# Performance work log

Measured on AMD Instinct MI355X. Metric: run time of the kernel, lower is better.

The kernel has to match this reference:

```python
import jax, jax.numpy as jnp
import numpy as np

EMB = 512
H = 8
DK = EMB // H          # 64
MAX_SEQ = 768
TOPK = MAX_SEQ // 2    # 384


def setup_inputs() -> dict:
    key = jax.random.key(0)
    ks = jax.random.split(key, 16)
    B, S, E = 1, MAX_SEQ, EMB

    def w(k, shape):
        return jax.random.normal(k, shape, dtype=jnp.float32) * 0.02

    return {
        "x": jax.random.normal(ks[0], (B, S, E), dtype=jnp.float32),
        # main attention projections (Linear weights stored as (in, out))
        "Wq": w(ks[1], (E, E)), "bq": w(ks[2], (E,)),
        "Wk": w(ks[3], (E, E)), "bk": w(ks[4], (E,)),
        "Wv": w(ks[5], (E, E)), "bv": w(ks[6], (E,)),
        "Wo": w(ks[7], (E, E)), "bo": w(ks[8], (E,)),
        # indexer projections: wq -> (E, H*DK)=(E,E), wk -> (E, DK), weights_proj -> (E, H)
        "iq_W": w(ks[9], (E, H * DK)), "iq_b": w(ks[10], (H * DK,)),
        "ik_W": w(ks[11], (E, DK)),    "ik_b": w(ks[12], (DK,)),
        "wp_W": w(ks[13], (E, H)),     "wp_b": w(ks[14], (H,)),
    }


def reference(x, Wq, bq, Wk, bk, Wv, bv, Wo, bo, iq_W, iq_b, ik_W, ik_b, wp_W, wp_b):
    B, S, E = x.shape
    scaling = 1.0 / np.sqrt(DK)

    def split_heads(z):  # (B,S,E) -> (B,H,S,DK)
        return z.reshape(B, S, H, DK).transpose(0, 2, 1, 3)

    Q = split_heads(x @ Wq + bq)
    K = split_heads(x @ Wk + bk)
    V = split_heads(x @ Wv + bv)

    # --- indexer: per-token relevance scores ---
    q_idx = (x @ iq_W + iq_b).reshape(B, S, H, DK).transpose(0, 2, 1, 3)  # (B,H,S,DK)
    k_idx = x @ ik_W + ik_b                                               # (B,S,DK)
    w_idx = x @ wp_W + wp_b                                               # (B,S,H)
    score = jax.nn.relu(jnp.einsum('bhsd,btd->bhst', q_idx, k_idx))       # (B,H,S,S)
    indexer_score = jnp.einsum('bhst,bsh->bst', score, w_idx)             # (B,S,S)

    # --- top-k selection (set-equivalent to argpartition in the original) ---
    topk_idx = jax.lax.top_k(indexer_score, TOPK)[1]                      # (B,S,TOPK) int32

    # --- gather sparse K/V per query token ---
    def gather_b(Zb, idxb):  # Zb:(H,S,DK), idxb:(S,TOPK) -> (H,S,TOPK,DK)
        return Zb[:, idxb, :]
    K_s = jax.vmap(gather_b)(K, topk_idx)  # (B,H,S,TOPK,DK)
    V_s = jax.vmap(gather_b)(V, topk_idx)  # (B,H,S,TOPK,DK)

    # --- sparse attention over selected tokens ---
    sc = jnp.einsum('bhsd,bhskd->bhsk', Q, K_s) * scaling  # (B,H,S,TOPK)
    wts = jax.nn.softmax(sc, axis=-1)
    attn = jnp.einsum('bhsk,bhskd->bhsd', wts, V_s)        # (B,H,S,DK)

    out = attn.transpose(0, 2, 1, 3).reshape(B, S, E) @ Wo + bo
    return out
```

## Files before the change

kernel.cpp:

```cpp
#include <hip/hip_runtime.h>
#include <hip/hip_bf16.h>
#include <math.h>

#define S 768
#define E 512
#define H 8
#define DK 64
#define TOPK 384

typedef short bf16x8 __attribute__((ext_vector_type(8)));
typedef float f32x4 __attribute__((ext_vector_type(4)));

__device__ __forceinline__ unsigned short f2bf(float x) {
  unsigned u = __float_as_uint(x);
  unsigned r = u + 0x7FFFu + ((u >> 16) & 1u);
  return (unsigned short)(r >> 16);
}
__device__ __forceinline__ float bf2f(unsigned short h) {
  return __uint_as_float(((unsigned)h) << 16);
}
__device__ __forceinline__ void split1(float x, unsigned short& h, unsigned short& l) {
  h = f2bf(x);
  l = f2bf(x - bf2f(h));
}

__device__ __forceinline__ void mfma3(f32x4& d, bf16x8 ah, bf16x8 al,
                                      bf16x8 bh, bf16x8 bl) {
  d = __builtin_amdgcn_mfma_f32_16x16x32_bf16(ah, bh, d, 0, 0, 0);
  d = __builtin_amdgcn_mfma_f32_16x16x32_bf16(ah, bl, d, 0, 0, 0);
  d = __builtin_amdgcn_mfma_f32_16x16x32_bf16(al, bh, d, 0, 0, 0);
}
__device__ __forceinline__ void mfma2(f32x4& d, bf16x8 ah, bf16x8 al, bf16x8 bh) {
  d = __builtin_amdgcn_mfma_f32_16x16x32_bf16(ah, bh, d, 0, 0, 0);
  d = __builtin_amdgcn_mfma_f32_16x16x32_bf16(al, bh, d, 0, 0, 0);
}

__device__ __forceinline__ bf16x8 ldfrag(const unsigned short* p) {
  return *reinterpret_cast<const bf16x8*>(p);
}

struct PrepTab {
  const float* src[8];
  unsigned short* hi[8];
  unsigned short* lo[8];
};

__global__ __launch_bounds__(256) void prep_kernel(PrepTab t) {
  const int seg = blockIdx.z;
  const int rows = (seg == 0) ? 768 : 512;
  const int cols = (seg == 5) ? 64 : ((seg == 6) ? 8 : 512);
  const int tx = (seg == 6) ? 2 : ((cols + 31) >> 5);
  const int ty = rows >> 5;
  if ((int)blockIdx.x >= tx || (int)blockIdx.y >= ty) return;
  const int r0 = blockIdx.y * 32, c0 = blockIdx.x * 32;
  const int tid = threadIdx.x;
  const int rl = tid >> 3, c4 = (tid & 7) << 2;
  const float* src = t.src[seg];
  if (seg == 0) {
    float4 v = *(const float4*)(src + (size_t)(r0 + rl) * cols + c0 + c4);
    unsigned short h[4], l[4];
    split1(v.x, h[0], l[0]); split1(v.y, h[1], l[1]);
    split1(v.z, h[2], l[2]); split1(v.w, h[3], l[3]);
    size_t off = (size_t)(r0 + rl) * cols + c0 + c4;
    *(ushort4*)(t.hi[seg] + off) = make_ushort4(h[0], h[1], h[2], h[3]);
    *(ushort4*)(t.lo[seg] + off) = make_ushort4(l[0], l[1], l[2], l[3]);
  } else {
    __shared__ float ts[32][33];
    #pragma unroll
    for (int j = 0; j < 4; ++j) {
      int c = c4 + j;
      ts[rl][c] = (c0 + c < cols) ? src[(size_t)(r0 + rl) * cols + c0 + c] : 0.0f;
    }
    __syncthreads();
    float v0 = ts[c4 + 0][rl], v1 = ts[c4 + 1][rl];
    float v2 = ts[c4 + 2][rl], v3 = ts[c4 + 3][rl];
    unsigned short h[4], l[4];
    split1(v0, h[0], l[0]); split1(v1, h[1], l[1]);
    split1(v2, h[2], l[2]); split1(v3, h[3], l[3]);
    size_t off = (size_t)(c0 + rl) * 512 + r0 + c4;
    *(ushort4*)(t.hi[seg] + off) = make_ushort4(h[0], h[1], h[2], h[3]);
    *(ushort4*)(t.lo[seg] + off) = make_ushort4(l[0], l[1], l[2], l[3]);
  }
}

struct ProjTab {
  const unsigned short* whi[6];
  const unsigned short* wlo[6];
  const float* bias[6];
};

__global__ __launch_bounds__(256) void proj_mfma_kernel(
    const unsigned short* __restrict__ Xhi, const unsigned short* __restrict__ Xlo,
    ProjTab pt,
    unsigned short* __restrict__ Qhi, unsigned short* __restrict__ Qlo,
    unsigned short* __restrict__ Khi, unsigned short* __restrict__ Klo,
    unsigned short* __restrict__ VThi,
    unsigned short* __restrict__ QIhi, unsigned short* __restrict__ QIlo,
    unsigned short* __restrict__ KIhi, unsigned short* __restrict__ KIlo,
    float* __restrict__ WI) {
  __shared__ __align__(16) unsigned short Ah[64][72];
  __shared__ __align__(16) unsigned short Al[64][72];
  __shared__ __align__(16) unsigned short Bh[64][72];
  __shared__ __align__(16) unsigned short Bl[64][72];
  const int bx = blockIdx.x;
  int seg, nt;
  if (bx < 32) { seg = bx >> 3; nt = bx & 7; }
  else         { seg = 4 + (bx - 32); nt = 0; }
  const int m0 = blockIdx.y * 64;
  const int n0 = nt * 64;
  const int tid = threadIdx.x;
  const int lane = tid & 63;
  const int wave = tid >> 6;
  const int mq = (wave >> 1) << 5;
  const int nq = (wave & 1) << 5;
  const int l15 = lane & 15;
  const int q8 = (lane >> 4) << 3;
  const int q4 = (lane >> 4) << 2;
  const unsigned short* Whi = pt.whi[seg];
  const unsigned short* Wlo = pt.wlo[seg];

  const int mm0 = tid >> 3,          kc0 = (tid & 7) << 3;
  const int mm1 = (tid + 256) >> 3,  kc1 = ((tid + 256) & 7) << 3;
  const size_t ga0 = (size_t)(m0 + mm0) * 512 + kc0;
  const size_t gb0 = (size_t)(n0 + mm0) * 512 + kc0;
  const size_t ga1 = (size_t)(m0 + mm1) * 512 + kc1;
  const size_t gb1 = (size_t)(n0 + mm1) * 512 + kc1;

  bf16x8 rah0 = ldfrag(Xhi + ga0), ral0 = ldfrag(Xlo + ga0);
  bf16x8 rbh0 = ldfrag(Whi + gb0), rbl0 = ldfrag(Wlo + gb0);
  bf16x8 rah1 = ldfrag(Xhi + ga1), ral1 = ldfrag(Xlo + ga1);
  bf16x8 rbh1 = ldfrag(Whi + gb1), rbl1 = ldfrag(Wlo + gb1);

  f32x4 acc[2][2] = {};
  for (int cc = 0; cc < 8; ++cc) {
    *(bf16x8*)&Ah[mm0][kc0] = rah0;
    *(bf16x8*)&Al[mm0][kc0] = ral0;
    *(bf16x8*)&Bh[mm0][kc0] = rbh0;
    *(bf16x8*)&Bl[mm0][kc0] = rbl0;
    *(bf16x8*)&Ah[mm1][kc1] = rah1;
    *(bf16x8*)&Al[mm1][kc1] = ral1;
    *(bf16x8*)&Bh[mm1][kc1] = rbh1;
    *(bf16x8*)&Bl[mm1][kc1] = rbl1;
    if (cc < 7) {
      const size_t o = (size_t)(cc + 1) << 6;
      rah0 = ldfrag(Xhi + ga0 + o); ral0 = ldfrag(Xlo + ga0 + o);
      rbh0 = ldfrag(Whi + gb0 + o); rbl0 = ldfrag(Wlo + gb0 + o);
      rah1 = ldfrag(Xhi + ga1 + o); ral1 = ldfrag(Xlo + ga1 + o);
      rbh1 = ldfrag(Whi + gb1 + o); rbl1 = ldfrag(Wlo + gb1 + o);
    }
    __syncthreads();
    #pragma unroll
    for (int ki = 0; ki < 64; ki += 32) {
      const int kk = ki + q8;
      bf16x8 ah0 = *(const bf16x8*)&Ah[mq + l15][kk];
      bf16x8 al0 = *(const bf16x8*)&Al[mq + l15][kk];
      bf16x8 ah1 = *(const bf16x8*)&Ah[mq + 16 + l15][kk];
      bf16x8 al1 = *(const bf16x8*)&Al[mq + 16 + l15][kk];
      bf16x8 bh0 = *(const bf16x8*)&Bh[nq + l15][kk];
      bf16x8 bl0 = *(const bf16x8*)&Bl[nq + l15][kk];
      bf16x8 bh1 = *(const bf16x8*)&Bh[nq + 16 + l15][kk];
      bf16x8 bl1 = *(const bf16x8*)&Bl[nq + 16 + l15][kk];
      mfma3(acc[0][0], ah0, al0, bh0, bl0);
      mfma3(acc[0][1], ah0, al0, bh1, bl1);
      mfma3(acc[1][0], ah1, al1, bh0, bl0);
      mfma3(acc[1][1], ah1, al1, bh1, bl1);
    }
    __syncthreads();
  }

  const float* bias = pt.bias[seg];
  #pragma unroll
  for (int ntt = 0; ntt < 2; ++ntt) {
    const int nloc = n0 + nq + ntt * 16 + l15;
    const float bv = (seg == 5 && nloc >= 8) ? 0.0f : bias[nloc];
    #pragma unroll
    for (int mt = 0; mt < 2; ++mt) {
      #pragma unroll
      for (int r = 0; r < 4; ++r) {
        const int m = m0 + mq + mt * 16 + q4 + r;
        const float v = acc[mt][ntt][r] + bv;
        unsigned short h16, l16;
        if (seg == 0) {
          split1(v, h16, l16);
          Qhi[(size_t)m * 512 + nloc] = h16;
          Qlo[(size_t)m * 512 + nloc] = l16;
        } else if (seg == 1) {
          const int hh = nloc >> 6, dd = nloc & 63;
          split1(v, h16, l16);
          Khi[((size_t)hh * S + m) * 64 + dd] = h16;
          Klo[((size_t)hh * S + m) * 64 + dd] = l16;
        } else if (seg == 2) {
          VThi[((size_t)(nloc >> 6) * 64 + (nloc & 63)) * S + m] = f2bf(v);
        } else if (seg == 3) {
          split1(v, h16, l16);
          QIhi[(size_t)m * 512 + nloc] = h16;
          QIlo[(size_t)m * 512 + nloc] = l16;
        } else if (seg == 4) {
          split1(v, h16, l16);
          KIhi[(size_t)m * 64 + nloc] = h16;
          KIlo[(size_t)m * 64 + nloc] = l16;
        } else {
          if (nloc < 8) WI[(size_t)m * 8 + nloc] = v;
        }
      }
    }
  }
}

__global__ __launch_bounds__(256) void indexer_mfma_kernel(
    const unsigned short* __restrict__ QIhi, const unsigned short* __restrict__ QIlo,
    const unsigned short* __restrict__ KIhi, const unsigned short* __restrict__ KIlo,
    const float* __restrict__ WI, float* __restrict__ ISC) {
  __shared__ __align__(16) unsigned short Qh[32][136];
  __shared__ __align__(16) unsigned short Ql[32][136];
  __shared__ float wis[32][8];
  const int s0 = blockIdx.y * 32, t0 = blockIdx.x * 64;
  const int tid = threadIdx.x;
  const int lane = tid & 63;
  const int wave = tid >> 6;
  const int mq = (wave >> 1) << 4;
  const int nqb = (wave & 1) << 5;
  const int l15 = lane & 15;
  const int q8 = (lane >> 4) << 3;
  const int q4 = (lane >> 4) << 2;
  wis[tid >> 3][tid & 7] = WI[(size_t)(s0 + (tid >> 3)) * 8 + (tid & 7)];

  const size_t brow0 = (size_t)(t0 + nqb + l15) * 64;
  const size_t brow1 = (size_t)(t0 + nqb + 16 + l15) * 64;
  bf16x8 kfh[2][2], kfl[2][2];
  #pragma unroll
  for (int kk = 0; kk < 2; ++kk) {
    const int kb = kk * 32 + q8;
    kfh[kk][0] = ldfrag(KIhi + brow0 + kb);
    kfl[kk][0] = ldfrag(KIlo + brow0 + kb);
    kfh[kk][1] = ldfrag(KIhi + brow1 + kb);
    kfl[kk][1] = ldfrag(KIlo + brow1 + kb);
  }

  const int smm = tid >> 3;
  const int skc = (tid & 7) << 4;
  const size_t qbase = (size_t)(s0 + smm) * 512 + skc;
  bf16x8 rq0 = ldfrag(QIhi + qbase);
  bf16x8 rq1 = ldfrag(QIhi + qbase + 8);
  bf16x8 rq2 = ldfrag(QIlo + qbase);
  bf16x8 rq3 = ldfrag(QIlo + qbase + 8);

  float accI[2][4] = {};
  for (int hp = 0; hp < 4; ++hp) {
    __syncthreads();
    *(bf16x8*)&Qh[smm][skc]     = rq0;
    *(bf16x8*)&Qh[smm][skc + 8] = rq1;
    *(bf16x8*)&Ql[smm][skc]     = rq2;
    *(bf16x8*)&Ql[smm][skc + 8] = rq3;
    if (hp < 3) {
      const size_t g = qbase + (size_t)(hp + 1) * 128;
      rq0 = ldfrag(QIhi + g);
      rq1 = ldfrag(QIhi + g + 8);
      rq2 = ldfrag(QIlo + g);
      rq3 = ldfrag(QIlo + g + 8);
    }
    __syncthreads();
    #pragma unroll
    for (int hh = 0; hh < 2; ++hh) {
      const int h = hp * 2 + hh;
      f32x4 d[2] = {};
      #pragma unroll
      for (int kk = 0; kk < 2; ++kk) {
        const int ka = hh * 64 + kk * 32 + q8;
        bf16x8 ah = *(const bf16x8*)&Qh[mq + l15][ka];
        bf16x8 al = *(const bf16x8*)&Ql[mq + l15][ka];
        mfma3(d[0], ah, al, kfh[kk][0], kfl[kk][0]);
        mfma3(d[1], ah, al, kfh[kk][1], kfl[kk][1]);
      }
      #pragma unroll
      for (int r = 0; r < 4; ++r) {
        const float w = wis[mq + q4 + r][h];
        accI[0][r] = fmaf(fmaxf(d[0][r], 0.0f), w, accI[0][r]);
        accI[1][r] = fmaf(fmaxf(d[1][r], 0.0f), w, accI[1][r]);
      }
    }
  }
  #pragma unroll
  for (int ntt = 0; ntt < 2; ++ntt)
    #pragma unroll
    for (int r = 0; r < 4; ++r)
      ISC[(size_t)(s0 + mq + q4 + r) * S + t0 + nqb + ntt * 16 + l15] = accI[ntt][r];
}

__global__ __launch_bounds__(256) void topk_kernel(
    const float* __restrict__ ISC, unsigned* __restrict__ Mask,
    float* __restrict__ Sum, float* __restrict__ ATTacc) {
  __shared__ unsigned ordv[768];
  __shared__ int hist[256];
  __shared__ int gsum[16];
  __shared__ int sc[256];
  __shared__ unsigned mw[24];
  __shared__ unsigned sh_prefix;
  __shared__ int sh_R;
  const int s = blockIdx.x;
  const int tid = threadIdx.x;
  for (int i = tid; i < 768; i += 256) {
    float f = ISC[s * 768 + i] + 0.0f;
    unsigned u = __float_as_uint(f);
    ordv[i] = (u & 0x80000000u) ? ~u : (u | 0x80000000u);
  }
  {
    const float4 z4 = {0.0f, 0.0f, 0.0f, 0.0f};
    if (tid < 128) *(float4*)(ATTacc + (size_t)s * 512 + tid * 4) = z4;
  }
  if (tid < 24) mw[tid] = 0u;
  if (tid < H) Sum[tid * S + s] = 0.0f;
  if (tid == 0) { sh_prefix = 0u; sh_R = TOPK; }
  __syncthreads();
  for (int pass = 0; pass < 4; ++pass) {
    const int shift = 24 - pass * 8;
    hist[tid] = 0;
    __syncthreads();
    const unsigned pm = (pass == 0) ? 0u : (0xFFFFFFFFu << (shift + 8));
    const unsigned pref = sh_prefix;
    for (int i = tid; i < 768; i += 256) {
      unsigned o = ordv[i];
      if ((o & pm) == pref) atomicAdd(&hist[(o >> shift) & 255], 1);
    }
    __syncthreads();
    if (tid < 16) {
      int t = 0;
      #pragma unroll
      for (int k = 0; k < 16; ++k) t += hist[tid * 16 + k];
      gsum[tid] = t;
    }
    __syncthreads();
    if (tid == 0) {
      int R = sh_R;
      int G = 0;
      int g = 15;
      for (; g > 0; --g) {
        if (G + gsum[g] >= R) break;
        G += gsum[g];
      }
      int b = 15;
      for (; b > 0; --b) {
        int c = hist[g * 16 + b];
        if (G + c >= R) break;
        G += c;
      }
      sh_prefix = sh_prefix | ((unsigned)(g * 16 + b) << shift);
      sh_R = R - G;
    }
    __syncthreads();
  }
  const unsigned thr = sh_prefix;
  const int need_eq = sh_R;
  const int base = tid * 3;
  unsigned o0 = ordv[base], o1 = ordv[base + 1], o2 = ordv[base + 2];
  int c = (o0 == thr) + (o1 == thr) + (o2 == thr);
  sc[tid] = c;
  __syncthreads();
  for (int off = 1; off < 256; off <<= 1) {
    int v = (tid >= off) ? sc[tid - off] : 0;
    __syncthreads();
    sc[tid] += v;
    __syncthreads();
  }
  int rank = sc[tid] - c;
  if (o0 > thr || (o0 == thr && rank < need_eq))
    atomicOr(&mw[base >> 5], 1u << (base & 31));
  if (o0 == thr) ++rank;
  if (o1 > thr || (o1 == thr && rank < need_eq))
    atomicOr(&mw[(base + 1) >> 5], 1u << ((base + 1) & 31));
  if (o1 == thr) ++rank;
  if (o2 > thr || (o2 == thr && rank < need_eq))
    atomicOr(&mw[(base + 2) >> 5], 1u << ((base + 2) & 31));
  __syncthreads();
  if (tid < 24) Mask[s * 24 + tid] = mw[tid];
}

__global__ __launch_bounds__(512) void sattn_kernel(
    const unsigned short* __restrict__ Qhi, const unsigned short* __restrict__ Qlo,
    const unsigned short* __restrict__ Khi, const unsigned short* __restrict__ Klo,
    const unsigned short* __restrict__ VThi,
    const unsigned* __restrict__ Mask, float* __restrict__ ATTacc,
    float* __restrict__ Sum) {
  __shared__ __align__(16) unsigned short Ksh[64][72];
  __shared__ __align__(16) unsigned short Ksl[64][72];
  __shared__ __align__(16) unsigned short Vsh[64][72];
  __shared__ __align__(16) unsigned short Pshi[64][72];
  __shared__ __align__(16) unsigned short Pslo[64][72];
  __shared__ unsigned msk[64][6];
  __shared__ float rsumf[64];
  const int ks = blockIdx.x;
  const int s0 = blockIdx.y * 64;
  const int h  = blockIdx.z;
  const int tid = threadIdx.x;
  const int lane = tid & 63;
  const int wave = tid >> 6;
  const int l15 = lane & 15;
  const int q8 = (lane >> 4) << 3;
  const int q4 = (lane >> 4) << 2;
  const int mq = (wave >> 1) << 4;
  const int nqq = (wave & 1) << 4;
  const int db = (wave & 1) << 5;

  if (tid < 384) msk[tid & 63][tid >> 6] =
      Mask[(size_t)(s0 + (tid & 63)) * 24 + ks * 6 + (tid >> 6)];
  if (tid < 64) rsumf[tid] = 0.0f;

  const size_t qrow = (size_t)(s0 + mq + l15) * 512 + h * 64;
  bf16x8 qh0 = ldfrag(Qhi + qrow + 0 + q8);
  bf16x8 ql0 = ldfrag(Qlo + qrow + 0 + q8);
  bf16x8 qh1 = ldfrag(Qhi + qrow + 32 + q8);
  bf16x8 ql1 = ldfrag(Qlo + qrow + 32 + q8);

  const int tr = tid >> 3;
  const int kc = (tid & 7) << 3;
  const size_t gkbase = ((size_t)h * S + ks * 192 + tr) * 64 + kc;
  const size_t gvbase = ((size_t)h * 64 + tr) * S + ks * 192 + kc;
  bf16x8 rkh = ldfrag(Khi + gkbase);
  bf16x8 rkl = ldfrag(Klo + gkbase);
  bf16x8 rv  = ldfrag(VThi + gvbase);

  f32x4 oacc[2] = {};
  for (int ct = 0; ct < 3; ++ct) {
    __syncthreads();
    *(bf16x8*)&Ksh[tr][kc] = rkh;
    *(bf16x8*)&Ksl[tr][kc] = rkl;
    *(bf16x8*)&Vsh[tr][kc] = rv;
    if (ct < 2) {
      rkh = ldfrag(Khi + gkbase + (size_t)(ct + 1) * 4096);
      rkl = ldfrag(Klo + gkbase + (size_t)(ct + 1) * 4096);
      rv  = ldfrag(VThi + gvbase + (size_t)(ct + 1) * 64);
    }
    __syncthreads();
    float esum[4] = {0.0f, 0.0f, 0.0f, 0.0f};
    #pragma unroll
    for (int cp = 0; cp < 2; ++cp) {
      const int tcol = nqq + cp * 32;
      f32x4 d = {0.0f, 0.0f, 0.0f, 0.0f};
      bf16x8 bh0 = *(const bf16x8*)&Ksh[tcol + l15][q8];
      bf16x8 bl0 = *(const bf16x8*)&Ksl[tcol + l15][q8];
      bf16x8 bh1 = *(const bf16x8*)&Ksh[tcol + l15][32 + q8];
      bf16x8 bl1 = *(const bf16x8*)&Ksl[tcol + l15][32 + q8];
      mfma3(d, qh0, ql0, bh0, bl0);
      mfma3(d, qh1, ql1, bh1, bl1);
      const int tl = ct * 64 + tcol + l15;
      #pragma unroll
      for (int r = 0; r < 4; ++r) {
        const int srow = mq + q4 + r;
        const unsigned w = msk[srow][tl >> 5];
        float e = ((w >> (tl & 31)) & 1u) ? __expf(d[r] * 0.125f) : 0.0f;
        unsigned short h16, l16;
        split1(e, h16, l16);
        Pshi[srow][tcol + l15] = h16;
        Pslo[srow][tcol + l15] = l16;
        esum[r] += e;
      }
    }
    float v0 = esum[0], v1 = esum[1], v2 = esum[2], v3 = esum[3];
    #pragma unroll
    for (int off = 1; off < 16; off <<= 1) {
      v0 += __shfl_xor(v0, off);
      v1 += __shfl_xor(v1, off);
      v2 += __shfl_xor(v2, off);
      v3 += __shfl_xor(v3, off);
    }
    if (l15 == 0) {
      atomicAdd(&rsumf[mq + q4 + 0], v0);
      atomicAdd(&rsumf[mq + q4 + 1], v1);
      atomicAdd(&rsumf[mq + q4 + 2], v2);
      atomicAdd(&rsumf[mq + q4 + 3], v3);
    }
    __syncthreads();
    #pragma unroll
    for (int kk = 0; kk < 64; kk += 32) {
      bf16x8 pah = *(const bf16x8*)&Pshi[mq + l15][kk + q8];
      bf16x8 pal = *(const bf16x8*)&Pslo[mq + l15][kk + q8];
      #pragma unroll
      for (int dt = 0; dt < 2; ++dt) {
        bf16x8 vbh = *(const bf16x8*)&Vsh[db + dt * 16 + l15][kk + q8];
        mfma2(oacc[dt], pah, pal, vbh);
      }
    }
  }
  #pragma unroll
  for (int dt = 0; dt < 2; ++dt) {
    const int dd = db + dt * 16 + l15;
    #pragma unroll
    for (int r = 0; r < 4; ++r) {
      const int s = s0 + mq + q4 + r;
      atomicAdd(&ATTacc[(size_t)s * E + h * DK + dd], oacc[dt][r]);
    }
  }
  __syncthreads();
  if (tid < 64) atomicAdd(&Sum[(size_t)h * S + s0 + tid], rsumf[tid]);
}

__global__ __launch_bounds__(512) void out_mfma_kernel(
    const float* __restrict__ ATTacc, const float* __restrict__ Sum,
    const unsigned short* __restrict__ WoThi,
    const float* __restrict__ bo, float* __restrict__ out) {
  __shared__ float AccL[16][65];
  __shared__ float ivs[16][8];
  __shared__ __align__(16) unsigned short Ahi[16][520];
  __shared__ __align__(16) unsigned short Alo[16][520];
  const int tid512 = threadIdx.x;
  const int wave8 = tid512 >> 6;
  const int z = wave8 >> 2;
  const int wave = wave8 & 3;
  const int lane = tid512 & 63;
  const int m0 = blockIdx.y * 16;
  const int n0 = blockIdx.x * 64 + wave * 16;
  const int l15 = lane & 15;
  const int q8 = (lane >> 4) << 3;
  const int q4 = (lane >> 4) << 2;
  if (tid512 < 128) {
    const int r = tid512 >> 3, hh = tid512 & 7;
    ivs[r][hh] = 1.0f / Sum[(size_t)hh * S + m0 + r];
  }
  __syncthreads();
  {
    const int row = tid512 >> 5;
    const int kb = (tid512 & 31) << 4;
    const float inv = ivs[row][kb >> 6];
    const float* src = ATTacc + (size_t)(m0 + row) * 512 + kb;
    float4 a0 = *(const float4*)(src);
    float4 a1 = *(const float4*)(src + 4);
    float4 a2 = *(const float4*)(src + 8);
    float4 a3 = *(const float4*)(src + 12);
    float v[16] = {a0.x, a0.y, a0.z, a0.w, a1.x, a1.y, a1.z, a1.w,
                   a2.x, a2.y, a2.z, a2.w, a3.x, a3.y, a3.z, a3.w};
    #pragma unroll
    for (int i = 0; i < 16; ++i) {
      unsigned short hh, ll;
      split1(v[i] * inv, hh, ll);
      Ahi[row][kb + i] = hh;
      Alo[row][kb + i] = ll;
    }
  }
  __syncthreads();
  const size_t brow = (size_t)(n0 + l15) * 512;
  f32x4 acc = {};
  #pragma unroll
  for (int it = 0; it < 8; ++it) {
    const int ko = (z << 8) + (it << 5) + q8;
    bf16x8 ah = *(const bf16x8*)&Ahi[l15][ko];
    bf16x8 al = *(const bf16x8*)&Alo[l15][ko];
    bf16x8 bh = ldfrag(WoThi + brow + ko);
    mfma2(acc, ah, al, bh);
  }
  if (z == 1) {
    #pragma unroll
    for (int r = 0; r < 4; ++r)
      AccL[q4 + r][wave * 16 + l15] = acc[r];
  }
  __syncthreads();
  if (z == 0) {
    const int n = n0 + l15;
    const float bv = bo[n];
    #pragma unroll
    for (int r = 0; r < 4; ++r)
      out[(size_t)(m0 + q4 + r) * 512 + n] =
          acc[r] + AccL[q4 + r][wave * 16 + l15] + bv;
  }
}

extern "C" void kernel_launch(void* const* d_in, const int* in_sizes, int n_in,
                              void* d_out, int out_size, void* d_ws, size_t ws_size,
                              hipStream_t stream) {
  const float* x    = (const float*)d_in[0];
  const float* Wq   = (const float*)d_in[1];
  const float* bq   = (const float*)d_in[2];
  const float* Wk   = (const float*)d_in[3];
  const float* bk   = (const float*)d_in[4];
  const float* Wv   = (const float*)d_in[5];
  const float* bv   = (const float*)d_in[6];
  const float* Wo   = (const float*)d_in[7];
  const float* bo   = (const float*)d_in[8];
  const float* iqW  = (const float*)d_in[9];
  const float* iqb  = (const float*)d_in[10];
  const float* ikW  = (const float*)d_in[11];
  const float* ikb  = (const float*)d_in[12];
  const float* wpW  = (const float*)d_in[13];
  const float* wpb  = (const float*)d_in[14];

  float* ws = (float*)d_ws;
  float* WI   = ws;
  float* ISC  = WI + S * H;
  unsigned* Mask = (unsigned*)(ISC + S * S);
  float* Sum  = (float*)(Mask + S * 24);
  float* ATTacc = Sum + H * S;
  unsigned short* u = (unsigned short*)(ATTacc + S * E);
  unsigned short* Xhi  = u;             u += S * E;
  unsigned short* Xlo  = u;             u += S * E;
  unsigned short* Qhi  = u;             u += S * E;
  unsigned short* Qlo  = u;             u += S * E;
  unsigned short* Khi  = u;             u += S * E;
  unsigned short* Klo  = u;             u += S * E;
  unsigned short* VThi = u;             u += S * E;
  unsigned short* QIhi = u;             u += S * E;
  unsigned short* QIlo = u;             u += S * E;
  unsigned short* KIhi = u;             u += S * DK;
  unsigned short* KIlo = u;             u += S * DK;
  unsigned short* WTq_hi = u;           u += E * E;
  unsigned short* WTk_hi = u;           u += E * E;
  unsigned short* WTv_hi = u;           u += E * E;
  unsigned short* WTiq_hi = u;          u += E * E;
  unsigned short* WTik_hi = u;          u += 64 * E;
  unsigned short* WTwp_hi = u;          u += 64 * E;
  unsigned short* WTo_hi = u;           u += E * E;
  unsigned short* WTq_lo = u;           u += E * E;
  unsigned short* WTk_lo = u;           u += E * E;
  unsigned short* WTv_lo = u;           u += E * E;
  unsigned short* WTiq_lo = u;          u += E * E;
  unsigned short* WTik_lo = u;          u += 64 * E;
  unsigned short* WTwp_lo = u;          u += 64 * E;
  unsigned short* WTo_lo = u;           u += E * E;

  PrepTab prep;
  prep.src[0] = x;    prep.hi[0] = Xhi;     prep.lo[0] = Xlo;
  prep.src[1] = Wq;   prep.hi[1] = WTq_hi;  prep.lo[1] = WTq_lo;
  prep.src[2] = Wk;   prep.hi[2] = WTk_hi;  prep.lo[2] = WTk_lo;
  prep.src[3] = Wv;   prep.hi[3] = WTv_hi;  prep.lo[3] = WTv_lo;
  prep.src[4] = iqW;  prep.hi[4] = WTiq_hi; prep.lo[4] = WTiq_lo;
  prep.src[5] = ikW;  prep.hi[5] = WTik_hi; prep.lo[5] = WTik_lo;
  prep.src[6] = wpW;  prep.hi[6] = WTwp_hi; prep.lo[6] = WTwp_lo;
  prep.src[7] = Wo;   prep.hi[7] = WTo_hi;  prep.lo[7] = WTo_lo;

  ProjTab pt;
  pt.whi[0] = WTq_hi;  pt.wlo[0] = WTq_lo;  pt.bias[0] = bq;
  pt.whi[1] = WTk_hi;  pt.wlo[1] = WTk_lo;  pt.bias[1] = bk;
  pt.whi[2] = WTv_hi;  pt.wlo[2] = WTv_lo;  pt.bias[2] = bv;
  pt.whi[3] = WTiq_hi; pt.wlo[3] = WTiq_lo; pt.bias[3] = iqb;
  pt.whi[4] = WTik_hi; pt.wlo[4] = WTik_lo; pt.bias[4] = ikb;
  pt.whi[5] = WTwp_hi; pt.wlo[5] = WTwp_lo; pt.bias[5] = wpb;

  prep_kernel<<<dim3(16, 24, 8), dim3(256), 0, stream>>>(prep);
  proj_mfma_kernel<<<dim3(34, S / 64), dim3(256), 0, stream>>>(
      Xhi, Xlo, pt, Qhi, Qlo, Khi, Klo, VThi, QIhi, QIlo, KIhi, KIlo, WI);
  indexer_mfma_kernel<<<dim3(S / 64, S / 32), dim3(256), 0, stream>>>(
      QIhi, QIlo, KIhi, KIlo, WI, ISC);
  topk_kernel<<<dim3(S), dim3(256), 0, stream>>>(ISC, Mask, Sum, ATTacc);
  sattn_kernel<<<dim3(4, S / 64, H), dim3(512), 0, stream>>>(
      Qhi, Qlo, Khi, Klo, VThi, Mask, ATTacc, Sum);
  out_mfma_kernel<<<dim3(8, 48), dim3(512), 0, stream>>>(
      ATTacc, Sum, WTo_hi, bo, (float*)d_out);
}
```

Measured before the change: 139.5 us.

## Double-buffer LDS tiles, use wave-shuffle scan, and load K/V fragments directly

The projection and indexer kernels now double-buffer their shared-memory tiles, which cuts one barrier per k-step and lets global prefetch run further ahead. The top-k rank scan replaces a barrier-heavy shared-memory Hillis-Steele scan with per-wave shuffle scans plus a small cross-wave combine. The sparse attention kernel drops its LDS staging of K and V, loads MFMA fragments straight from global memory, double-buffers the P tile, and defers the row-sum reduction to the end. The price is more LDS per block in some kernels and uncoalesced direct global loads in the attention kernel.

Result: slower. 147.0 us (+5.3%).

```diff
diff --git a/kernel.cpp b/kernel.cpp
--- a/kernel.cpp
+++ b/kernel.cpp
@@ -98,10 +98,10 @@
     unsigned short* __restrict__ QIhi, unsigned short* __restrict__ QIlo,
     unsigned short* __restrict__ KIhi, unsigned short* __restrict__ KIlo,
     float* __restrict__ WI) {
-  __shared__ __align__(16) unsigned short Ah[64][72];
-  __shared__ __align__(16) unsigned short Al[64][72];
-  __shared__ __align__(16) unsigned short Bh[64][72];
-  __shared__ __align__(16) unsigned short Bl[64][72];
+  __shared__ __align__(16) unsigned short Ah[2][64][72];
+  __shared__ __align__(16) unsigned short Al[2][64][72];
+  __shared__ __align__(16) unsigned short Bh[2][64][72];
+  __shared__ __align__(16) unsigned short Bl[2][64][72];
   const int bx = blockIdx.x;
   int seg, nt;
   if (bx < 32) { seg = bx >> 3; nt = bx & 7; }
@@ -130,36 +130,44 @@
   bf16x8 rbh0 = ldfrag(Whi + gb0), rbl0 = ldfrag(Wlo + gb0);
   bf16x8 rah1 = ldfrag(Xhi + ga1), ral1 = ldfrag(Xlo + ga1);
   bf16x8 rbh1 = ldfrag(Whi + gb1), rbl1 = ldfrag(Wlo + gb1);
+  *(bf16x8*)&Ah[0][mm0][kc0] = rah0;  *(bf16x8*)&Al[0][mm0][kc0] = ral0;
+  *(bf16x8*)&Bh[0][mm0][kc0] = rbh0;  *(bf16x8*)&Bl[0][mm0][kc0] = rbl0;
+  *(bf16x8*)&Ah[0][mm1][kc1] = rah1;  *(bf16x8*)&Al[0][mm1][kc1] = ral1;
+  *(bf16x8*)&Bh[0][mm1][kc1] = rbh1;  *(bf16x8*)&Bl[0][mm1][kc1] = rbl1;
+  rah0 = ldfrag(Xhi + ga0 + 64); ral0 = ldfrag(Xlo + ga0 + 64);
+  rbh0 = ldfrag(Whi + gb0 + 64); rbl0 = ldfrag(Wlo + gb0 + 64);
+  rah1 = ldfrag(Xhi + ga1 + 64); ral1 = ldfrag(Xlo + ga1 + 64);
+  rbh1 = ldfrag(Whi + gb1 + 64); rbl1 = ldfrag(Wlo + gb1 + 64);
+  __syncthreads();
 
   f32x4 acc[2][2] = {};
   for (int cc = 0; cc < 8; ++cc) {
-    *(bf16x8*)&Ah[mm0][kc0] = rah0;
-    *(bf16x8*)&Al[mm0][kc0] = ral0;
-    *(bf16x8*)&Bh[mm0][kc0] = rbh0;
-    *(bf16x8*)&Bl[mm0][kc0] = rbl0;
-    *(bf16x8*)&Ah[mm1][kc1] = rah1;
-    *(bf16x8*)&Al[mm1][kc1] = ral1;
-    *(bf16x8*)&Bh[mm1][kc1] = rbh1;
-    *(bf16x8*)&Bl[mm1][kc1] = rbl1;
+    const int cur = cc & 1;
     if (cc < 7) {
-      const size_t o = (size_t)(cc + 1) << 6;
+      const int nb = 1 - cur;
+      *(bf16x8*)&Ah[nb][mm0][kc0] = rah0;  *(bf16x8*)&Al[nb][mm0][kc0] = ral0;
+      *(bf16x8*)&Bh[nb][mm0][kc0] = rbh0;  *(bf16x8*)&Bl[nb][mm0][kc0] = rbl0;
+      *(bf16x8*)&Ah[nb][mm1][kc1] = rah1;  *(bf16x8*)&Al[nb][mm1][kc1] = ral1;
+      *(bf16x8*)&Bh[nb][mm1][kc1] = rbh1;  *(bf16x8*)&Bl[nb][mm1][kc1] = rbl1;
+    }
+    if (cc < 6) {
+      const size_t o = (size_t)(cc + 2) << 6;
       rah0 = ldfrag(Xhi + ga0 + o); ral0 = ldfrag(Xlo + ga0 + o);
       rbh0 = ldfrag(Whi + gb0 + o); rbl0 = ldfrag(Wlo + gb0 + o);
       rah1 = ldfrag(Xhi + ga1 + o); ral1 = ldfrag(Xlo + ga1 + o);
       rbh1 = ldfrag(Whi + gb1 + o); rbl1 = ldfrag(Wlo + gb1 + o);
     }
-    __syncthreads();
     #pragma unroll
     for (int ki = 0; ki < 64; ki += 32) {
       const int kk = ki + q8;
-      bf16x8 ah0 = *(const bf16x8*)&Ah[mq + l15][kk];
-      bf16x8 al0 = *(const bf16x8*)&Al[mq + l15][kk];
-      bf16x8 ah1 = *(const bf16x8*)&Ah[mq + 16 + l15][kk];
-      bf16x8 al1 = *(const bf16x8*)&Al[mq + 16 + l15][kk];
-      bf16x8 bh0 = *(const bf16x8*)&Bh[nq + l15][kk];
-      bf16x8 bl0 = *(const bf16x8*)&Bl[nq + l15][kk];
-      bf16x8 bh1 = *(const bf16x8*)&Bh[nq + 16 + l15][kk];
-      bf16x8 bl1 = *(const bf16x8*)&Bl[nq + 16 + l15][kk];
+      bf16x8 ah0 = *(const bf16x8*)&Ah[cur][mq + l15][kk];
+      bf16x8 al0 = *(const bf16x8*)&Al[cur][mq + l15][kk];
+      bf16x8 ah1 = *(const bf16x8*)&Ah[cur][mq + 16 + l15][kk];
+      bf16x8 al1 = *(const bf16x8*)&Al[cur][mq + 16 + l15][kk];
+      bf16x8 bh0 = *(const bf16x8*)&Bh[cur][nq + l15][kk];
+      bf16x8 bl0 = *(const bf16x8*)&Bl[cur][nq + l15][kk];
+      bf16x8 bh1 = *(const bf16x8*)&Bh[cur][nq + 16 + l15][kk];
+      bf16x8 bl1 = *(const bf16x8*)&Bl[cur][nq + 16 + l15][kk];
       mfma3(acc[0][0], ah0, al0, bh0, bl0);
       mfma3(acc[0][1], ah0, al0, bh1, bl1);
       mfma3(acc[1][0], ah1, al1, bh0, bl0);
@@ -211,8 +219,8 @@
     const unsigned short* __restrict__ QIhi, const unsigned short* __restrict__ QIlo,
     const unsigned short* __restrict__ KIhi, const unsigned short* __restrict__ KIlo,
     const float* __restrict__ WI, float* __restrict__ ISC) {
-  __shared__ __align__(16) unsigned short Qh[32][136];
-  __shared__ __align__(16) unsigned short Ql[32][136];
+  __shared__ __align__(16) unsigned short Qh[2][32][136];
+  __shared__ __align__(16) unsigned short Ql[2][32][136];
   __shared__ float wis[32][8];
   const int s0 = blockIdx.y * 32, t0 = blockIdx.x * 64;
   const int tid = threadIdx.x;
@@ -244,22 +252,33 @@
   bf16x8 rq1 = ldfrag(QIhi + qbase + 8);
   bf16x8 rq2 = ldfrag(QIlo + qbase);
   bf16x8 rq3 = ldfrag(QIlo + qbase + 8);
+  *(bf16x8*)&Qh[0][smm][skc]     = rq0;
+  *(bf16x8*)&Qh[0][smm][skc + 8] = rq1;
+  *(bf16x8*)&Ql[0][smm][skc]     = rq2;
+  *(bf16x8*)&Ql[0][smm][skc + 8] = rq3;
+  rq0 = ldfrag(QIhi + qbase + 128);
+  rq1 = ldfrag(QIhi + qbase + 136);
+  rq2 = ldfrag(QIlo + qbase + 128);
+  rq3 = ldfrag(QIlo + qbase + 136);
+  __syncthreads();
 
   float accI[2][4] = {};
   for (int hp = 0; hp < 4; ++hp) {
-    __syncthreads();
-    *(bf16x8*)&Qh[smm][skc]     = rq0;
-    *(bf16x8*)&Qh[smm][skc + 8] = rq1;
-    *(bf16x8*)&Ql[smm][skc]     = rq2;
-    *(bf16x8*)&Ql[smm][skc + 8] = rq3;
+    const int cur = hp & 1;
     if (hp < 3) {
-      const size_t g = qbase + (size_t)(hp + 1) * 128;
+      const int nb = 1 - cur;
+      *(bf16x8*)&Qh[nb][smm][skc]     = rq0;
+      *(bf16x8*)&Qh[nb][smm][skc + 8] = rq1;
+      *(bf16x8*)&Ql[nb][smm][skc]     = rq2;
+      *(bf16x8*)&Ql[nb][smm][skc + 8] = rq3;
+    }
+    if (hp < 2) {
+      const size_t g = qbase + (size_t)(hp + 2) * 128;
       rq0 = ldfrag(QIhi + g);
       rq1 = ldfrag(QIhi + g + 8);
       rq2 = ldfrag(QIlo + g);
       rq3 = ldfrag(QIlo + g + 8);
     }
-    __syncthreads();
     #pragma unroll
     for (int hh = 0; hh < 2; ++hh) {
       const int h = hp * 2 + hh;
@@ -267,8 +286,8 @@
       #pragma unroll
       for (int kk = 0; kk < 2; ++kk) {
         const int ka = hh * 64 + kk * 32 + q8;
-        bf16x8 ah = *(const bf16x8*)&Qh[mq + l15][ka];
-        bf16x8 al = *(const bf16x8*)&Ql[mq + l15][ka];
+        bf16x8 ah = *(const bf16x8*)&Qh[cur][mq + l15][ka];
+        bf16x8 al = *(const bf16x8*)&Ql[cur][mq + l15][ka];
         mfma3(d[0], ah, al, kfh[kk][0], kfl[kk][0]);
         mfma3(d[1], ah, al, kfh[kk][1], kfl[kk][1]);
       }
@@ -279,6 +298,7 @@
         accI[1][r] = fmaf(fmaxf(d[1][r], 0.0f), w, accI[1][r]);
       }
     }
+    __syncthreads();
   }
   #pragma unroll
   for (int ntt = 0; ntt < 2; ++ntt)
@@ -293,7 +313,7 @@
   __shared__ unsigned ordv[768];
   __shared__ int hist[256];
   __shared__ int gsum[16];
-  __shared__ int sc[256];
+  __shared__ int wtot[4];
   __shared__ unsigned mw[24];
   __shared__ unsigned sh_prefix;
   __shared__ int sh_R;
@@ -354,15 +374,19 @@
   const int base = tid * 3;
   unsigned o0 = ordv[base], o1 = ordv[base + 1], o2 = ordv[base + 2];
   int c = (o0 == thr) + (o1 == thr) + (o2 == thr);
-  sc[tid] = c;
-  __syncthreads();
-  for (int off = 1; off < 256; off <<= 1) {
-    int v = (tid >= off) ? sc[tid - off] : 0;
-    __syncthreads();
-    sc[tid] += v;
-    __syncthreads();
-  }
-  int rank = sc[tid] - c;
+  const int lane = tid & 63, wv = tid >> 6;
+  int sum = c;
+  #pragma unroll
+  for (int off = 1; off < 64; off <<= 1) {
+    int v = __shfl_up(sum, off);
+    if (lane >= off) sum += v;
+  }
+  if (lane == 63) wtot[wv] = sum;
+  __syncthreads();
+  int rank = sum - c;
+  if (wv > 0) rank += wtot[0];
+  if (wv > 1) rank += wtot[1];
+  if (wv > 2) rank += wtot[2];
   if (o0 > thr || (o0 == thr && rank < need_eq))
     atomicOr(&mw[base >> 5], 1u << (base & 31));
   if (o0 == thr) ++rank;
@@ -381,11 +405,8 @@
     const unsigned short* __restrict__ VThi,
     const unsigned* __restrict__ Mask, float* __restrict__ ATTacc,
     float* __restrict__ Sum) {
-  __shared__ __align__(16) unsigned short Ksh[64][72];
-  __shared__ __align__(16) unsigned short Ksl[64][72];
-  __shared__ __align__(16) unsigned short Vsh[64][72];
-  __shared__ __align__(16) unsigned short Pshi[64][72];
-  __shared__ __align__(16) unsigned short Pslo[64][72];
+  __shared__ __align__(16) unsigned short Pshi[2][64][72];
+  __shared__ __align__(16) unsigned short Pslo[2][64][72];
   __shared__ unsigned msk[64][6];
   __shared__ float rsumf[64];
   const int ks = blockIdx.x;
@@ -406,43 +427,38 @@
   if (tid < 64) rsumf[tid] = 0.0f;
 
   const size_t qrow = (size_t)(s0 + mq + l15) * 512 + h * 64;
-  bf16x8 qh0 = ldfrag(Qhi + qrow + 0 + q8);
-  bf16x8 ql0 = ldfrag(Qlo + qrow + 0 + q8);
+  bf16x8 qh0 = ldfrag(Qhi + qrow + q8);
+  bf16x8 ql0 = ldfrag(Qlo + qrow + q8);
   bf16x8 qh1 = ldfrag(Qhi + qrow + 32 + q8);
   bf16x8 ql1 = ldfrag(Qlo + qrow + 32 + q8);
 
-  const int tr = tid >> 3;
-  const int kc = (tid & 7) << 3;
-  const size_t gkbase = ((size_t)h * S + ks * 192 + tr) * 64 + kc;
-  const size_t gvbase = ((size_t)h * 64 + tr) * S + ks * 192 + kc;
-  bf16x8 rkh = ldfrag(Khi + gkbase);
-  bf16x8 rkl = ldfrag(Klo + gkbase);
-  bf16x8 rv  = ldfrag(VThi + gvbase);
-
+  const size_t kb0 = ((size_t)h * S + ks * 192 + nqq + l15) * 64 + q8;
+  const size_t vb0 = ((size_t)h * 64 + db + l15) * S + ks * 192 + q8;
+
+  float esum[4] = {0.0f, 0.0f, 0.0f, 0.0f};
   f32x4 oacc[2] = {};
+  __syncthreads();
+
+  #pragma unroll
   for (int ct = 0; ct < 3; ++ct) {
-    __syncthreads();
-    *(bf16x8*)&Ksh[tr][kc] = rkh;
-    *(bf16x8*)&Ksl[tr][kc] = rkl;
-    *(bf16x8*)&Vsh[tr][kc] = rv;
-    if (ct < 2) {
-      rkh = ldfrag(Khi + gkbase + (size_t)(ct + 1) * 4096);
-      rkl = ldfrag(Klo + gkbase + (size_t)(ct + 1) * 4096);
-      rv  = ldfrag(VThi + gvbase + (size_t)(ct + 1) * 64);
-    }
-    __syncthreads();
-    float esum[4] = {0.0f, 0.0f, 0.0f, 0.0f};
+    const int cur = ct & 1;
+    const int tch = ct * 64;
+    bf16x8 v00 = ldfrag(VThi + vb0 + tch);
+    bf16x8 v01 = ldfrag(VThi + vb0 + tch + 32);
+    bf16x8 v10 = ldfrag(VThi + vb0 + (size_t)16 * S + tch);
+    bf16x8 v11 = ldfrag(VThi + vb0 + (size_t)16 * S + tch + 32);
     #pragma unroll
     for (int cp = 0; cp < 2; ++cp) {
+      const size_t ka = kb0 + ((size_t)tch + cp * 32) * 64;
+      bf16x8 kh0 = ldfrag(Khi + ka);
+      bf16x8 kl0 = ldfrag(Klo + ka);
+      bf16x8 kh1 = ldfrag(Khi + ka + 32);
+      bf16x8 kl1 = ldfrag(Klo + ka + 32);
+      f32x4 d = {0.0f, 0.0f, 0.0f, 0.0f};
+      mfma3(d, qh0, ql0, kh0, kl0);
+      mfma3(d, qh1, ql1, kh1, kl1);
       const int tcol = nqq + cp * 32;
-      f32x4 d = {0.0f, 0.0f, 0.0f, 0.0f};
-      bf16x8 bh0 = *(const bf16x8*)&Ksh[tcol + l15][q8];
-      bf16x8 bl0 = *(const bf16x8*)&Ksl[tcol + l15][q8];
-      bf16x8 bh1 = *(const bf16x8*)&Ksh[tcol + l15][32 + q8];
-      bf16x8 bl1 = *(const bf16x8*)&Ksl[tcol + l15][32 + q8];
-      mfma3(d, qh0, ql0, bh0, bl0);
-      mfma3(d, qh1, ql1, bh1, bl1);
-      const int tl = ct * 64 + tcol + l15;
+      const int tl = tch + tcol + l15;
       #pragma unroll
       for (int r = 0; r < 4; ++r) {
         const int srow = mq + q4 + r;
@@ -450,36 +466,32 @@
         float e = ((w >> (tl & 31)) & 1u) ? __expf(d[r] * 0.125f) : 0.0f;
         unsigned short h16, l16;
         split1(e, h16, l16);
-        Pshi[srow][tcol + l15] = h16;
-        Pslo[srow][tcol + l15] = l16;
+        Pshi[cur][srow][tcol + l15] = h16;
+        Pslo[cur][srow][tcol + l15] = l16;
         esum[r] += e;
       }
     }
-    float v0 = esum[0], v1 = esum[1], v2 = esum[2], v3 = esum[3];
-    #pragma unroll
-    for (int off = 1; off < 16; off <<= 1) {
-      v0 += __shfl_xor(v0, off);
-      v1 += __shfl_xor(v1, off);
-      v2 += __shfl_xor(v2, off);
-      v3 += __shfl_xor(v3, off);
-    }
-    if (l15 == 0) {
-      atomicAdd(&rsumf[mq + q4 + 0], v0);
-      atomicAdd(&rsumf[mq + q4 + 1], v1);
-      atomicAdd(&rsumf[mq + q4 + 2], v2);
-      atomicAdd(&rsumf[mq + q4 + 3], v3);
-    }
     __syncthreads();
     #pragma unroll
     for (int kk = 0; kk < 64; kk += 32) {
-      bf16x8 pah = *(const bf16x8*)&Pshi[mq + l15][kk + q8];
-      bf16x8 pal = *(const bf16x8*)&Pslo[mq + l15][kk + q8];
-      #pragma unroll
-      for (int dt = 0; dt < 2; ++dt) {
-        bf16x8 vbh = *(const bf16x8*)&Vsh[db + dt * 16 + l15][kk + q8];
-        mfma2(oacc[dt], pah, pal, vbh);
-      }
-    }
+      bf16x8 pah = *(const bf16x8*)&Pshi[cur][mq + l15][kk + q8];
+      bf16x8 pal = *(const bf16x8*)&Pslo[cur][mq + l15][kk + q8];
+      mfma2(oacc[0], pah, pal, (kk == 0) ? v00 : v01);
+      mfma2(oacc[1], pah, pal, (kk == 0) ? v10 : v11);
+    }
+  }
+  #pragma unroll
+  for (int off = 1; off < 16; off <<= 1) {
+    esum[0] += __shfl_xor(esum[0], off);
+    esum[1] += __shfl_xor(esum[1], off);
+    esum[2] += __shfl_xor(esum[2], off);
+    esum[3] += __shfl_xor(esum[3], off);
+  }
+  if (l15 == 0) {
+    atomicAdd(&rsumf[mq + q4 + 0], esum[0]);
+    atomicAdd(&rsumf[mq + q4 + 1], esum[1]);
+    atomicAdd(&rsumf[mq + q4 + 2], esum[2]);
+    atomicAdd(&rsumf[mq + q4 + 3], esum[3]);
   }
   #pragma unroll
   for (int dt = 0; dt < 2; ++dt) {
```
